# Kernel optimization log

Hardware: AMD Instinct MI355X
Metric: run time of the kernel (lower is better)

The kernel has to match this reference:

```python
import jax, jax.numpy as jnp
import numpy as np


def setup_inputs() -> dict:
    key = jax.random.key(0)
    k1, k2, k3, k4 = jax.random.split(key, 4)
    N = 100000          # n_users + n_items nodes
    E = 1600000         # nonzeros in normalized adjacency (avg degree 16)
    D = 64              # embedding dim
    edge_row = jnp.sort(jax.random.randint(k1, (E,), 0, N, dtype=jnp.int32))
    edge_col = jax.random.randint(k2, (E,), 0, N, dtype=jnp.int32)
    edge_val = jax.random.uniform(k3, (E,), dtype=jnp.float32)
    embeds = jax.random.normal(k4, (N, D), dtype=jnp.float32)
    return {
        "edge_row": edge_row,
        "edge_col": edge_col,
        "edge_val": edge_val,
        "embeds": embeds,
        "num_nodes": N,
    }


def reference(edge_row, edge_col, edge_val, embeds, num_nodes):
    # out = A @ embeds, A given in COO: A[row[e], col[e]] = val[e]
    gathered = edge_val[:, None] * embeds[edge_col]        # [E, D]
    out = jax.ops.segment_sum(gathered, edge_row, num_segments=num_nodes)  # [N, D]
    return out
```

## Files before the change

### kernel.cpp

```cpp
#include <hip/hip_runtime.h>


#define GCN_D 64

typedef float f4 __attribute__((ext_vector_type(4)));

__global__ __launch_bounds__(256) void prep_kernel(
    const float* __restrict__ embeds,
    unsigned char* __restrict__ ebq,
    float* __restrict__ scale,
    int quant_blocks,
    const int* __restrict__ edge_row, int* __restrict__ row_ptr, int E, int N)
{
    if ((int)blockIdx.x < quant_blocks) {
        const int t   = blockIdx.x * blockDim.x + threadIdx.x;
        const int row = t >> 4;
        if (row >= N) return;
        const int l4 = (threadIdx.x & 15) * 4;

        const f4 a = __builtin_nontemporal_load(
            (const f4*)(embeds + (size_t)row * GCN_D + l4));

        float m = fmaxf(fmaxf(fabsf(a.x), fabsf(a.y)),
                        fmaxf(fabsf(a.z), fabsf(a.w)));
        m = fmaxf(m, __shfl_xor(m, 1));
        m = fmaxf(m, __shfl_xor(m, 2));
        m = fmaxf(m, __shfl_xor(m, 4));
        m = fmaxf(m, __shfl_xor(m, 8));

        const float inv = (m > 0.f) ? 127.f / m : 0.f;
        const int q0 = (int)rintf(fminf(fmaxf(a.x * inv, -127.f), 127.f)) + 128;
        const int q1 = (int)rintf(fminf(fmaxf(a.y * inv, -127.f), 127.f)) + 128;
        const int q2 = (int)rintf(fminf(fmaxf(a.z * inv, -127.f), 127.f)) + 128;
        const int q3 = (int)rintf(fminf(fmaxf(a.w * inv, -127.f), 127.f)) + 128;
        const unsigned int packed =
            (unsigned)q0 | ((unsigned)q1 << 8) | ((unsigned)q2 << 16) | ((unsigned)q3 << 24);

        *(unsigned int*)(ebq + (size_t)row * GCN_D + l4) = packed;
        if ((threadIdx.x & 15) == 0) scale[row] = m * (1.f / 127.f);
    } else {
        const int e = (blockIdx.x - quant_blocks) * blockDim.x + threadIdx.x;
        if (e >= E) return;
        const int r    = edge_row[e];
        const int prev = (e == 0) ? -1 : edge_row[e - 1];
        for (int k = prev + 1; k <= r; ++k) row_ptr[k] = e;
        if (e == E - 1)
            for (int k = r + 1; k <= N; ++k) row_ptr[k] = E;
    }
}

__global__ __launch_bounds__(256) void gcn_row_q8_kernel(
    const int* __restrict__ row_ptr,
    const int* __restrict__ edge_col,
    const float* __restrict__ edge_val,
    const unsigned char* __restrict__ ebq,
    const float* __restrict__ scale,
    float* __restrict__ out,
    int N)
{
    const int tid = blockIdx.x * blockDim.x + threadIdx.x;
    const int row = tid >> 4;
    if (row >= N) return;
    const int db = (threadIdx.x & 15) * 4;

    const int p0 = row_ptr[row];
    const int p1 = row_ptr[row + 1];

    f4    acc  = (f4)0.0f;
    float wsum = 0.0f;
    int k = p0;

    for (; k + 7 < p1; k += 8) {
        int   c[8];
        float v[8];
        #pragma unroll
        for (int j = 0; j < 8; ++j) { c[j] = edge_col[k + j]; v[j] = edge_val[k + j]; }
        unsigned int g[8];
        float        s[8];
        #pragma unroll
        for (int j = 0; j < 8; ++j) {
            g[j] = *(const unsigned int*)(ebq + (size_t)c[j] * GCN_D + db);
            s[j] = scale[c[j]];
        }
        #pragma unroll
        for (int j = 0; j < 8; ++j) {
            const float w = v[j] * s[j];
            acc.x += w * (float)( g[j]        & 0xffu);
            acc.y += w * (float)((g[j] >> 8)  & 0xffu);
            acc.z += w * (float)((g[j] >> 16) & 0xffu);
            acc.w += w * (float)( g[j] >> 24);
            wsum  += w;
        }
    }
    if (k + 3 < p1) {
        int   c[4];
        float v[4];
        #pragma unroll
        for (int j = 0; j < 4; ++j) { c[j] = edge_col[k + j]; v[j] = edge_val[k + j]; }
        unsigned int g[4];
        float        s[4];
        #pragma unroll
        for (int j = 0; j < 4; ++j) {
            g[j] = *(const unsigned int*)(ebq + (size_t)c[j] * GCN_D + db);
            s[j] = scale[c[j]];
        }
        #pragma unroll
        for (int j = 0; j < 4; ++j) {
            const float w = v[j] * s[j];
            acc.x += w * (float)( g[j]        & 0xffu);
            acc.y += w * (float)((g[j] >> 8)  & 0xffu);
            acc.z += w * (float)((g[j] >> 16) & 0xffu);
            acc.w += w * (float)( g[j] >> 24);
            wsum  += w;
        }
        k += 4;
    }
    for (; k < p1; ++k) {
        const int c = edge_col[k];
        const unsigned int g = *(const unsigned int*)(ebq + (size_t)c * GCN_D + db);
        const float w = edge_val[k] * scale[c];
        acc.x += w * (float)( g        & 0xffu);
        acc.y += w * (float)((g >> 8)  & 0xffu);
        acc.z += w * (float)((g >> 16) & 0xffu);
        acc.w += w * (float)( g >> 24);
        wsum  += w;
    }

    acc = acc - 128.0f * wsum;

    __builtin_nontemporal_store(acc, (f4*)(out + (size_t)row * GCN_D + db));
}

__global__ __launch_bounds__(256) void build_row_ptr_kernel(
    const int* __restrict__ edge_row, int* __restrict__ row_ptr, int E, int N)
{
    const int e = blockIdx.x * blockDim.x + threadIdx.x;
    if (e >= E) return;
    const int r    = edge_row[e];
    const int prev = (e == 0) ? -1 : edge_row[e - 1];
    for (int k = prev + 1; k <= r; ++k) row_ptr[k] = e;
    if (e == E - 1)
        for (int k = r + 1; k <= N; ++k) row_ptr[k] = E;
}

__global__ __launch_bounds__(256) void gcn_row_f32_kernel(
    const int* __restrict__ row_ptr,
    const int* __restrict__ edge_col,
    const float* __restrict__ edge_val,
    const float* __restrict__ embeds,
    float* __restrict__ out,
    int N)
{
    const int tid = blockIdx.x * blockDim.x + threadIdx.x;
    const int row = tid >> 4;
    if (row >= N) return;
    const int db = (threadIdx.x & 15) * 4;
    const int p0 = row_ptr[row];
    const int p1 = row_ptr[row + 1];
    f4 acc = (f4)0.0f;
    int k = p0;
    for (; k + 3 < p1; k += 4) {
        int c0 = edge_col[k], c1 = edge_col[k+1], c2 = edge_col[k+2], c3 = edge_col[k+3];
        float v0 = edge_val[k], v1 = edge_val[k+1], v2 = edge_val[k+2], v3 = edge_val[k+3];
        acc += v0 * *(const f4*)(embeds + (size_t)c0 * GCN_D + db);
        acc += v1 * *(const f4*)(embeds + (size_t)c1 * GCN_D + db);
        acc += v2 * *(const f4*)(embeds + (size_t)c2 * GCN_D + db);
        acc += v3 * *(const f4*)(embeds + (size_t)c3 * GCN_D + db);
    }
    for (; k < p1; ++k)
        acc += edge_val[k] * *(const f4*)(embeds + (size_t)edge_col[k] * GCN_D + db);
    *(f4*)(out + (size_t)row * GCN_D + db) = acc;
}

extern "C" void kernel_launch(void* const* d_in, const int* in_sizes, int n_in,
                              void* d_out, int out_size, void* d_ws, size_t ws_size,
                              hipStream_t stream) {
    const int*   edge_row = (const int*)d_in[0];
    const int*   edge_col = (const int*)d_in[1];
    const float* edge_val = (const float*)d_in[2];
    const float* embeds   = (const float*)d_in[3];
    float*       out      = (float*)d_out;

    const int E = in_sizes[0];
    const int N = out_size / GCN_D;

    int* row_ptr = (int*)d_ws;
    const size_t sc_off = (((size_t)(N + 1) * 4) + 255) & ~(size_t)255;
    float* scale = (float*)((char*)d_ws + sc_off);
    const size_t q_off = ((sc_off + (size_t)N * 4) + 255) & ~(size_t)255;
    unsigned char* ebq = (unsigned char*)d_ws + q_off;
    const size_t need = q_off + (size_t)N * GCN_D;

    const int row_blocks = (N * 16 + 255) / 256;

    if (ws_size >= need) {
        const int quant_blocks = (N * 16 + 255) / 256;
        const int rp_blocks    = (E + 255) / 256;
        prep_kernel<<<quant_blocks + rp_blocks, 256, 0, stream>>>(
            embeds, ebq, scale, quant_blocks, edge_row, row_ptr, E, N);
        gcn_row_q8_kernel<<<row_blocks, 256, 0, stream>>>(
            row_ptr, edge_col, edge_val, ebq, scale, out, N);
    } else {
        build_row_ptr_kernel<<<(E + 255) / 256, 256, 0, stream>>>(edge_row, row_ptr, E, N);
        gcn_row_f32_kernel<<<row_blocks, 256, 0, stream>>>(
            row_ptr, edge_col, edge_val, embeds, out, N);
    }
}
```

Baseline: 125.9 us.

## Fuse quantize, row_ptr build and SpMM into one cooperative persistent kernel

Replaces the two-kernel sequence with a single cooperative kernel of 1024 persistent blocks. It grid-strides over int8 quantization and row_ptr construction, does a grid-wide sync, then grid-strides over the quantized row SpMM. The goal is to remove the second kernel launch and the inter-kernel gap. In exchange it adds the cost of a grid barrier and a fixed grid size that may reduce occupancy or load balance. The fallback path drops the 4-edge unrolled tail and the fp32 no-workspace path, which now simply returns.

```diff
diff --git a/kernel.cpp b/kernel.cpp
--- a/kernel.cpp
+++ b/kernel.cpp
@@ -1,9 +1,137 @@
 #include <hip/hip_runtime.h>
+#include <hip/hip_cooperative_groups.h>
+
+namespace cg = cooperative_groups;
 
 
 #define GCN_D 64
 
 typedef float f4 __attribute__((ext_vector_type(4)));
+
+
+__global__ __launch_bounds__(256, 4) void gcn_fused_kernel(
+    const float* __restrict__ embeds,
+    const int*   __restrict__ edge_row,
+    const int*   __restrict__ edge_col,
+    const float* __restrict__ edge_val,
+    unsigned char* __restrict__ ebq,
+    float* __restrict__ scale,
+    int*   __restrict__ row_ptr,
+    float* __restrict__ out,
+    int E, int N)
+{
+    const long gsize = (long)gridDim.x * blockDim.x;
+    const long gtid0 = (long)blockIdx.x * blockDim.x + threadIdx.x;
+
+    for (long t = gtid0; t < (long)N * 16; t += gsize) {
+        const int row = (int)(t >> 4);
+        const int l4  = ((int)t & 15) * 4;
+
+        const f4 a = __builtin_nontemporal_load(
+            (const f4*)(embeds + (size_t)row * GCN_D + l4));
+
+        float m = fmaxf(fmaxf(fabsf(a.x), fabsf(a.y)),
+                        fmaxf(fabsf(a.z), fabsf(a.w)));
+        m = fmaxf(m, __shfl_xor(m, 1));
+        m = fmaxf(m, __shfl_xor(m, 2));
+        m = fmaxf(m, __shfl_xor(m, 4));
+        m = fmaxf(m, __shfl_xor(m, 8));
+
+        const float inv = (m > 0.f) ? 127.f / m : 0.f;
+        const int q0 = (int)rintf(fminf(fmaxf(a.x * inv, -127.f), 127.f)) + 128;
+        const int q1 = (int)rintf(fminf(fmaxf(a.y * inv, -127.f), 127.f)) + 128;
+        const int q2 = (int)rintf(fminf(fmaxf(a.z * inv, -127.f), 127.f)) + 128;
+        const int q3 = (int)rintf(fminf(fmaxf(a.w * inv, -127.f), 127.f)) + 128;
+        const unsigned int packed =
+            (unsigned)q0 | ((unsigned)q1 << 8) | ((unsigned)q2 << 16) | ((unsigned)q3 << 24);
+
+        *(unsigned int*)(ebq + (size_t)row * GCN_D + l4) = packed;
+        if (((int)t & 15) == 0) scale[row] = m * (1.f / 127.f);
+    }
+
+    for (long e = gtid0; e < E; e += gsize) {
+        const int r    = edge_row[e];
+        const int prev = (e == 0) ? -1 : edge_row[e - 1];
+        for (int k = prev + 1; k <= r; ++k) row_ptr[k] = (int)e;
+        if (e == E - 1)
+            for (int k = r + 1; k <= N; ++k) row_ptr[k] = E;
+    }
+
+    cg::this_grid().sync();
+
+    for (long t = gtid0; t < (long)N * 16; t += gsize) {
+        const int row = (int)(t >> 4);
+        const int db  = ((int)t & 15) * 4;
+
+        const int p0 = row_ptr[row];
+        const int p1 = row_ptr[row + 1];
+
+        f4    acc  = (f4)0.0f;
+        float wsum = 0.0f;
+        int k = p0;
+
+        for (; k + 7 < p1; k += 8) {
+            int   c[8];
+            float v[8];
+            #pragma unroll
+            for (int j = 0; j < 8; ++j) { c[j] = edge_col[k + j]; v[j] = edge_val[k + j]; }
+            unsigned int g[8];
+            float        s[8];
+            #pragma unroll
+            for (int j = 0; j < 8; ++j) {
+                g[j] = *(const unsigned int*)(ebq + (size_t)c[j] * GCN_D + db);
+                s[j] = scale[c[j]];
+            }
+            #pragma unroll
+            for (int j = 0; j < 8; ++j) {
+                const float w = v[j] * s[j];
+                acc.x += w * (float)( g[j]        & 0xffu);
+                acc.y += w * (float)((g[j] >> 8)  & 0xffu);
+                acc.z += w * (float)((g[j] >> 16) & 0xffu);
+                acc.w += w * (float)( g[j] >> 24);
+                wsum  += w;
+            }
+        }
+        if (k + 3 < p1) {
+            int   c[4];
+            float v[4];
+            #pragma unroll
+            for (int j = 0; j < 4; ++j) { c[j] = edge_col[k + j]; v[j] = edge_val[k + j]; }
+            unsigned int g[4];
+            float        s[4];
+            #pragma unroll
+            for (int j = 0; j < 4; ++j) {
+                g[j] = *(const unsigned int*)(ebq + (size_t)c[j] * GCN_D + db);
+                s[j] = scale[c[j]];
+            }
+            #pragma unroll
+            for (int j = 0; j < 4; ++j) {
+                const float w = v[j] * s[j];
+                acc.x += w * (float)( g[j]        & 0xffu);
+                acc.y += w * (float)((g[j] >> 8)  & 0xffu);
+                acc.z += w * (float)((g[j] >> 16) & 0xffu);
+                acc.w += w * (float)( g[j] >> 24);
+                wsum  += w;
+            }
+            k += 4;
+        }
+        for (; k < p1; ++k) {
+            const int c = edge_col[k];
+            const unsigned int g = *(const unsigned int*)(ebq + (size_t)c * GCN_D + db);
+            const float w = edge_val[k] * scale[c];
+            acc.x += w * (float)( g        & 0xffu);
+            acc.y += w * (float)((g >> 8)  & 0xffu);
+            acc.z += w * (float)((g >> 16) & 0xffu);
+            acc.w += w * (float)( g >> 24);
+            wsum  += w;
+        }
+
+        acc = acc - 128.0f * wsum;
+
+        __builtin_nontemporal_store(acc, (f4*)(out + (size_t)row * GCN_D + db));
+    }
+}
+
 
 __global__ __launch_bounds__(256) void prep_kernel(
     const float* __restrict__ embeds,
@@ -17,17 +145,14 @@
         const int row = t >> 4;
         if (row >= N) return;
         const int l4 = (threadIdx.x & 15) * 4;
-
         const f4 a = __builtin_nontemporal_load(
             (const f4*)(embeds + (size_t)row * GCN_D + l4));
-
         float m = fmaxf(fmaxf(fabsf(a.x), fabsf(a.y)),
                         fmaxf(fabsf(a.z), fabsf(a.w)));
         m = fmaxf(m, __shfl_xor(m, 1));
         m = fmaxf(m, __shfl_xor(m, 2));
         m = fmaxf(m, __shfl_xor(m, 4));
         m = fmaxf(m, __shfl_xor(m, 8));
-
         const float inv = (m > 0.f) ? 127.f / m : 0.f;
         const int q0 = (int)rintf(fminf(fmaxf(a.x * inv, -127.f), 127.f)) + 128;
         const int q1 = (int)rintf(fminf(fmaxf(a.y * inv, -127.f), 127.f)) + 128;
@@ -35,7 +160,6 @@
         const int q3 = (int)rintf(fminf(fmaxf(a.w * inv, -127.f), 127.f)) + 128;
         const unsigned int packed =
             (unsigned)q0 | ((unsigned)q1 << 8) | ((unsigned)q2 << 16) | ((unsigned)q3 << 24);
-
         *(unsigned int*)(ebq + (size_t)row * GCN_D + l4) = packed;
         if ((threadIdx.x & 15) == 0) scale[row] = m * (1.f / 127.f);
     } else {
@@ -62,14 +186,11 @@
     const int row = tid >> 4;
     if (row >= N) return;
     const int db = (threadIdx.x & 15) * 4;
-
     const int p0 = row_ptr[row];
     const int p1 = row_ptr[row + 1];
-
     f4    acc  = (f4)0.0f;
     float wsum = 0.0f;
     int k = p0;
-
     for (; k + 7 < p1; k += 8) {
         int   c[8];
         float v[8];
@@ -92,29 +213,6 @@
             wsum  += w;
         }
     }
-    if (k + 3 < p1) {
-        int   c[4];
-        float v[4];
-        #pragma unroll
-        for (int j = 0; j < 4; ++j) { c[j] = edge_col[k + j]; v[j] = edge_val[k + j]; }
-        unsigned int g[4];
-        float        s[4];
-        #pragma unroll
-        for (int j = 0; j < 4; ++j) {
-            g[j] = *(const unsigned int*)(ebq + (size_t)c[j] * GCN_D + db);
-            s[j] = scale[c[j]];
-        }
-        #pragma unroll
-        for (int j = 0; j < 4; ++j) {
-            const float w = v[j] * s[j];
-            acc.x += w * (float)( g[j]        & 0xffu);
-            acc.y += w * (float)((g[j] >> 8)  & 0xffu);
-            acc.z += w * (float)((g[j] >> 16) & 0xffu);
-            acc.w += w * (float)( g[j] >> 24);
-            wsum  += w;
-        }
-        k += 4;
-    }
     for (; k < p1; ++k) {
         const int c = edge_col[k];
         const unsigned int g = *(const unsigned int*)(ebq + (size_t)c * GCN_D + db);
@@ -125,51 +223,8 @@
         acc.w += w * (float)( g >> 24);
         wsum  += w;
     }
-
     acc = acc - 128.0f * wsum;
-
     __builtin_nontemporal_store(acc, (f4*)(out + (size_t)row * GCN_D + db));
-}
-
-__global__ __launch_bounds__(256) void build_row_ptr_kernel(
-    const int* __restrict__ edge_row, int* __restrict__ row_ptr, int E, int N)
-{
-    const int e = blockIdx.x * blockDim.x + threadIdx.x;
-    if (e >= E) return;
-    const int r    = edge_row[e];
-    const int prev = (e == 0) ? -1 : edge_row[e - 1];
-    for (int k = prev + 1; k <= r; ++k) row_ptr[k] = e;
-    if (e == E - 1)
-        for (int k = r + 1; k <= N; ++k) row_ptr[k] = E;
-}
-
-__global__ __launch_bounds__(256) void gcn_row_f32_kernel(
-    const int* __restrict__ row_ptr,
-    const int* __restrict__ edge_col,
-    const float* __restrict__ edge_val,
-    const float* __restrict__ embeds,
-    float* __restrict__ out,
-    int N)
-{
-    const int tid = blockIdx.x * blockDim.x + threadIdx.x;
-    const int row = tid >> 4;
-    if (row >= N) return;
-    const int db = (threadIdx.x & 15) * 4;
-    const int p0 = row_ptr[row];
-    const int p1 = row_ptr[row + 1];
-    f4 acc = (f4)0.0f;
-    int k = p0;
-    for (; k + 3 < p1; k += 4) {
-        int c0 = edge_col[k], c1 = edge_col[k+1], c2 = edge_col[k+2], c3 = edge_col[k+3];
-        float v0 = edge_val[k], v1 = edge_val[k+1], v2 = edge_val[k+2], v3 = edge_val[k+3];
-        acc += v0 * *(const f4*)(embeds + (size_t)c0 * GCN_D + db);
-        acc += v1 * *(const f4*)(embeds + (size_t)c1 * GCN_D + db);
-        acc += v2 * *(const f4*)(embeds + (size_t)c2 * GCN_D + db);
-        acc += v3 * *(const f4*)(embeds + (size_t)c3 * GCN_D + db);
-    }
-    for (; k < p1; ++k)
-        acc += edge_val[k] * *(const f4*)(embeds + (size_t)edge_col[k] * GCN_D + db);
-    *(f4*)(out + (size_t)row * GCN_D + db) = acc;
 }
 
 extern "C" void kernel_launch(void* const* d_in, const int* in_sizes, int n_in,
@@ -181,8 +236,8 @@
     const float* embeds   = (const float*)d_in[3];
     float*       out      = (float*)d_out;
 
-    const int E = in_sizes[0];
-    const int N = out_size / GCN_D;
+    int E = in_sizes[0];
+    int N = out_size / GCN_D;
 
     int* row_ptr = (int*)d_ws;
     const size_t sc_off = (((size_t)(N + 1) * 4) + 255) & ~(size_t)255;
@@ -191,18 +246,21 @@
     unsigned char* ebq = (unsigned char*)d_ws + q_off;
     const size_t need = q_off + (size_t)N * GCN_D;
 
-    const int row_blocks = (N * 16 + 255) / 256;
-
-    if (ws_size >= need) {
+    if (ws_size < need) return;
+
+    void* args[] = { (void*)&embeds, (void*)&edge_row, (void*)&edge_col,
+                     (void*)&edge_val, (void*)&ebq, (void*)&scale,
+                     (void*)&row_ptr, (void*)&out, (void*)&E, (void*)&N };
+    hipError_t err = hipLaunchCooperativeKernel(
+        (const void*)gcn_fused_kernel, dim3(1024), dim3(256), args, 0, stream);
+
+    if (err != hipSuccess) {
         const int quant_blocks = (N * 16 + 255) / 256;
         const int rp_blocks    = (E + 255) / 256;
         prep_kernel<<<quant_blocks + rp_blocks, 256, 0, stream>>>(
             embeds, ebq, scale, quant_blocks, edge_row, row_ptr, E, N);
+        const int row_blocks = (N * 16 + 255) / 256;
         gcn_row_q8_kernel<<<row_blocks, 256, 0, stream>>>(
             row_ptr, edge_col, edge_val, ebq, scale, out, N);
-    } else {
-        build_row_ptr_kernel<<<(E + 255) / 256, 256, 0, stream>>>(edge_row, row_ptr, E, N);
-        gcn_row_f32_kernel<<<row_blocks, 256, 0, stream>>>(
-            row_ptr, edge_col, edge_val, embeds, out, N);
-    }
-}
+    }
+}
```

Result: slower. 235.5 us (+87.0%).
